# Performance work log

Measured on AMD Instinct MI355X. Metric: run time of the kernel, lower is better.

The kernel has to match this reference:

```python
import jax, jax.numpy as jnp
import numpy as np

# metaLinearLayer: per-sample weight W_b = left^T @ diag(meta_b) @ right.
# torch builds diag(meta)@eye@left then transposes and matmuls right, i.e.
# meta_weight[b] = (diag(meta_b) @ left).T @ right, shape (input_dim, out_dim).
# We apply it via associativity: (x @ left^T) * meta, then @ right -- same math,
# skipping the dense per-sample weight.

B, S, D_IN, D_OUT, P = 8, 4096, 2048, 2048, 256

def setup_inputs() -> dict:
    key = jax.random.key(0)
    ks = jax.random.split(key, 6)
    scale_l = (6.0 / D_IN) ** 0.5   # kaiming_uniform-ish magnitude
    scale_r = (6.0 / P) ** 0.5
    return {
        "input": jax.random.normal(ks[0], (B, S, D_IN), dtype=jnp.float32),
        "meta_input": jax.random.normal(ks[1], (B, P), dtype=jnp.float32),
        "left": jax.random.uniform(ks[2], (P, D_IN), dtype=jnp.float32, minval=-scale_l, maxval=scale_l),
        "right": jax.random.uniform(ks[3], (P, D_OUT), dtype=jnp.float32, minval=-scale_r, maxval=scale_r),
        "bias_w": jax.random.uniform(ks[4], (P, D_OUT), dtype=jnp.float32, minval=-scale_r, maxval=scale_r),
        "bias_b": jax.random.uniform(ks[5], (D_OUT,), dtype=jnp.float32, minval=-scale_r, maxval=scale_r),
    }

def reference(input, meta_input, left, right, bias_w, bias_b):
    # project input to rank-P space: [B,S,P]
    h = jnp.einsum('bsj,pj->bsp', input, left)
    # per-sample diagonal scaling by meta_input
    h = h * meta_input[:, None, :]
    # project to out_dim: [B,S,out_dim]
    out = jnp.einsum('bsp,pk->bsk', h, right)
    # meta bias = project2bias(meta_input), broadcast over seq
    meta_bias = meta_input @ bias_w + bias_b  # [B, out_dim]
    return out + meta_bias[:, None, :]
```

## Files before the change

### kernel.cpp

```cpp
#include <hip/hip_runtime.h>
#include <hip/hip_bf16.h>
#include <stdint.h>

#define B_    8
#define S_    4096
#define DIN   2048
#define DOUT  2048
#define P_    256
#define M_    (B_ * S_)

typedef __attribute__((ext_vector_type(4))) float f32x4;
typedef __attribute__((ext_vector_type(8))) short bf16x8;
typedef __attribute__((ext_vector_type(4))) short bf16x4;

static __device__ __forceinline__ short f2bs(float x) {
    __hip_bfloat16 h = __float2bfloat16(x);
    return *reinterpret_cast<short*>(&h);
}

static __device__ __forceinline__ void gld_lds16(const void* g, void* l) {
    __builtin_amdgcn_global_load_lds(
        (const __attribute__((address_space(1))) unsigned int*)(uintptr_t)g,
        (__attribute__((address_space(3))) unsigned int*)(uintptr_t)l,
        16, 0, 0);
}

#define SWZ(row, byteoff) ((byteoff) ^ (((row) & 7) << 4))

__global__ __launch_bounds__(256)
void cvt_left(const float* __restrict__ src, short* __restrict__ dst) {
    int i = blockIdx.x * 256 + threadIdx.x;
    const float4* s = reinterpret_cast<const float4*>(src) + (size_t)i * 2;
    float4 a = s[0], b = s[1];
    bf16x8 o;
    o[0]=f2bs(a.x); o[1]=f2bs(a.y); o[2]=f2bs(a.z); o[3]=f2bs(a.w);
    o[4]=f2bs(b.x); o[5]=f2bs(b.y); o[6]=f2bs(b.z); o[7]=f2bs(b.w);
    *(reinterpret_cast<bf16x8*>(dst) + i) = o;
}

__global__ __launch_bounds__(256)
void transposeR(const float* __restrict__ R, short* __restrict__ Rt) {
    __shared__ float T[64][65];
    const int n0 = blockIdx.x * 64;
    const int p0 = blockIdx.y * 64;
    const int tid = threadIdx.x;
    #pragma unroll
    for (int e = 0; e < 16; ++e) {
        int idx = tid + e * 256;
        int r = idx >> 6, c = idx & 63;
        T[r][c] = R[(size_t)(p0 + r) * DOUT + n0 + c];
    }
    __syncthreads();
    #pragma unroll
    for (int e = 0; e < 4; ++e) {
        int g = tid + e * 256;
        int n = g >> 4, p4 = (g & 15) << 2;
        bf16x4 v;
        v[0] = f2bs(T[p4 + 0][n]); v[1] = f2bs(T[p4 + 1][n]);
        v[2] = f2bs(T[p4 + 2][n]); v[3] = f2bs(T[p4 + 3][n]);
        *reinterpret_cast<bf16x4*>(&Rt[(size_t)(n0 + n) * P_ + p0 + p4]) = v;
    }
}

__global__ __launch_bounds__(256)
void meta_bias(const float* __restrict__ meta,
               const float* __restrict__ bias_w,
               const float* __restrict__ bias_b,
               float* __restrict__ mb) {
    int b = blockIdx.x >> 3;
    int k = (blockIdx.x & 7) * 256 + threadIdx.x;
    const float* mrow = meta + b * P_;
    float acc = bias_b[k];
    #pragma unroll 8
    for (int p = 0; p < P_; ++p)
        acc = fmaf(mrow[p], bias_w[(size_t)p * DOUT + k], acc);
    mb[(size_t)b * DOUT + k] = acc;
}

__global__ __launch_bounds__(256, 2)
void gemm1(const float* __restrict__ X, const short* __restrict__ Lb,
           const float* __restrict__ meta, char* __restrict__ Hsw) {
    __shared__ short As[2][64 * 64];

    const int tid  = threadIdx.x;
    const int lane = tid & 63;
    const int w    = tid >> 6;
    const int lm   = lane & 15;
    const int rg   = lane >> 4;
    const int mblk = blockIdx.x;
    const int r0   = mblk * 64;
    const int bidx = mblk >> 6;

    const int row_s = tid >> 2;
    const int kq    = (tid & 3) * 16;
    const float* xbase = X + (size_t)(r0 + row_s) * DIN + kq;
    const int wsw0 = SWZ(row_s, row_s * 128 + kq * 2);
    const int wsw1 = SWZ(row_s, row_s * 128 + kq * 2 + 16);

    f32x4 acc[4][4] = {};
    float4 xr0, xr1, xr2, xr3;
    {
        const float4* s = reinterpret_cast<const float4*>(xbase);
        xr0 = s[0]; xr1 = s[1]; xr2 = s[2]; xr3 = s[3];
    }

    for (int kt = 0; kt < 32; ++kt) {
        char* asb = (char*)As[kt & 1];
        bf16x8 o0, o1;
        o0[0]=f2bs(xr0.x); o0[1]=f2bs(xr0.y); o0[2]=f2bs(xr0.z); o0[3]=f2bs(xr0.w);
        o0[4]=f2bs(xr1.x); o0[5]=f2bs(xr1.y); o0[6]=f2bs(xr1.z); o0[7]=f2bs(xr1.w);
        o1[0]=f2bs(xr2.x); o1[1]=f2bs(xr2.y); o1[2]=f2bs(xr2.z); o1[3]=f2bs(xr2.w);
        o1[4]=f2bs(xr3.x); o1[5]=f2bs(xr3.y); o1[6]=f2bs(xr3.z); o1[7]=f2bs(xr3.w);
        *reinterpret_cast<bf16x8*>(asb + wsw0) = o0;
        *reinterpret_cast<bf16x8*>(asb + wsw1) = o1;
        __syncthreads();

        if (kt < 31) {
            const float4* s = reinterpret_cast<const float4*>(xbase + (kt + 1) * 64);
            xr0 = s[0]; xr1 = s[1]; xr2 = s[2]; xr3 = s[3];
        }

        bf16x8 bfr[4][2];
        #pragma unroll
        for (int j = 0; j < 4; ++j)
            #pragma unroll
            for (int kk = 0; kk < 2; ++kk)
                bfr[j][kk] = *reinterpret_cast<const bf16x8*>(
                    Lb + (size_t)(w * 64 + j * 16 + lm) * DIN + kt * 64 + kk * 32 + rg * 8);

        #pragma unroll
        for (int kk = 0; kk < 2; ++kk) {
            bf16x8 af[4];
            #pragma unroll
            for (int i = 0; i < 4; ++i) {
                int m = i * 16 + lm;
                af[i] = *reinterpret_cast<const bf16x8*>(
                    asb + SWZ(m, m * 128 + (kk * 32 + rg * 8) * 2));
            }
            #pragma unroll
            for (int i = 0; i < 4; ++i)
                #pragma unroll
                for (int j = 0; j < 4; ++j)
                    acc[i][j] = __builtin_amdgcn_mfma_f32_16x16x32_bf16(
                        af[i], bfr[j][kk], acc[i][j], 0, 0, 0);
        }
    }

    const float* mrow = meta + bidx * P_;
    char* hb = Hsw + (size_t)mblk * 32768 + w * 8192;
    float mv[4];
    #pragma unroll
    for (int j = 0; j < 4; ++j) mv[j] = mrow[w * 64 + j * 16 + lm];
    #pragma unroll
    for (int i = 0; i < 4; ++i) {
        #pragma unroll
        for (int j = 0; j < 4; ++j) {
            int kk2 = j * 16 + lm;
            #pragma unroll
            for (int q = 0; q < 4; ++q) {
                int r = i * 16 + rg * 4 + q;
                *reinterpret_cast<short*>(hb + SWZ(r, r * 128 + kk2 * 2)) =
                    f2bs(acc[i][j][q] * mv[j]);
            }
        }
    }
}

__global__ __launch_bounds__(256, 3)
void gemm2(const char* __restrict__ Hsw, const short* __restrict__ Rt,
           const float* __restrict__ mb, float* __restrict__ O) {
    __shared__ short As[64 * 64];

    const int tid  = threadIdx.x;
    const int lane = tid & 63;
    const int w    = tid >> 6;
    const int lm   = lane & 15;
    const int rg   = lane >> 4;
    const int mblk = blockIdx.x;
    const int r0   = mblk * 64;
    const int c0   = blockIdx.y * 256;
    const int bidx = mblk >> 6;
    char* asb = (char*)As;

    f32x4 acc[4][4] = {};

    for (int kt = 0; kt < 4; ++kt) {
        const char* aimg = Hsw + ((size_t)mblk * 4 + kt) * 8192;
        gld_lds16(aimg + (w * 2 + 0) * 1024 + lane * 16, asb + (w * 2 + 0) * 1024);
        gld_lds16(aimg + (w * 2 + 1) * 1024 + lane * 16, asb + (w * 2 + 1) * 1024);
        __syncthreads();

        bf16x8 bfr[4][2];
        #pragma unroll
        for (int j = 0; j < 4; ++j)
            #pragma unroll
            for (int kk = 0; kk < 2; ++kk)
                bfr[j][kk] = *reinterpret_cast<const bf16x8*>(
                    Rt + (size_t)(c0 + w * 64 + j * 16 + lm) * P_ + kt * 64 + kk * 32 + rg * 8);

        #pragma unroll
        for (int kk = 0; kk < 2; ++kk) {
            bf16x8 af[4];
            #pragma unroll
            for (int i = 0; i < 4; ++i) {
                int m = i * 16 + lm;
                af[i] = *reinterpret_cast<const bf16x8*>(
                    asb + SWZ(m, m * 128 + (kk * 32 + rg * 8) * 2));
            }
            #pragma unroll
            for (int i = 0; i < 4; ++i)
                #pragma unroll
                for (int j = 0; j < 4; ++j)
                    acc[i][j] = __builtin_amdgcn_mfma_f32_16x16x32_bf16(
                        af[i], bfr[j][kk], acc[i][j], 0, 0, 0);
        }
        __syncthreads();
    }

    const float* mbr = mb + (size_t)bidx * DOUT;
    float bv[4];
    #pragma unroll
    for (int j = 0; j < 4; ++j) bv[j] = mbr[c0 + w * 64 + j * 16 + lm];
    #pragma unroll
    for (int i = 0; i < 4; ++i) {
        #pragma unroll
        for (int j = 0; j < 4; ++j) {
            int col = c0 + w * 64 + j * 16 + lm;
            #pragma unroll
            for (int q = 0; q < 4; ++q) {
                int row = r0 + i * 16 + rg * 4 + q;
                O[(size_t)row * DOUT + col] = acc[i][j][q] + bv[j];
            }
        }
    }
}

extern "C" void kernel_launch(void* const* d_in, const int* in_sizes, int n_in,
                              void* d_out, int out_size, void* d_ws, size_t ws_size,
                              hipStream_t stream) {
    const float* input  = (const float*)d_in[0];
    const float* meta   = (const float*)d_in[1];
    const float* left   = (const float*)d_in[2];
    const float* right  = (const float*)d_in[3];
    const float* bias_w = (const float*)d_in[4];
    const float* bias_b = (const float*)d_in[5];
    float* out = (float*)d_out;

    char* ws  = (char*)d_ws;
    char* Hsw = ws;
    float* mb = (float*)(ws + 16777216);
    short* Lb = (short*)(ws + 16777216 + 65536);
    short* Rt = (short*)(ws + 16777216 + 65536 + 1048576);

    cvt_left  <<<256, 256, 0, stream>>>(left, Lb);
    transposeR<<<dim3(DOUT / 64, P_ / 64), 256, 0, stream>>>(right, Rt);
    meta_bias <<<64, 256, 0, stream>>>(meta, bias_w, bias_b, mb);

    gemm1<<<dim3(M_ / 64), 256, 0, stream>>>(input, Lb, meta, Hsw);
    gemm2<<<dim3(M_ / 64, DOUT / 256), 256, 0, stream>>>(Hsw, Rt, mb, out);
}
```

Baseline: 597.0 us.

## Fuse both GEMMs into one kernel keeping H in LDS, prepack weights as fragments

Merges gemm1 and gemm2 into a single kernel. Each 64-row block keeps its scaled rank-256 intermediate H in shared memory and then loops over all 2048 output columns, so H is no longer written to and read back from global memory. The left and right weights are pre-packed into MFMA fragment order so each lane's B-operand loads are contiguous. The trade-offs are fewer blocks (512 instead of 4096 for the second stage), 48KB of LDS per block, and a serial loop over the 8 output tiles.

```diff
diff --git a/kernel.cpp b/kernel.cpp
--- a/kernel.cpp
+++ b/kernel.cpp
@@ -11,35 +11,33 @@
 
 typedef __attribute__((ext_vector_type(4))) float f32x4;
 typedef __attribute__((ext_vector_type(8))) short bf16x8;
-typedef __attribute__((ext_vector_type(4))) short bf16x4;
 
 static __device__ __forceinline__ short f2bs(float x) {
     __hip_bfloat16 h = __float2bfloat16(x);
     return *reinterpret_cast<short*>(&h);
 }
 
-static __device__ __forceinline__ void gld_lds16(const void* g, void* l) {
-    __builtin_amdgcn_global_load_lds(
-        (const __attribute__((address_space(1))) unsigned int*)(uintptr_t)g,
-        (__attribute__((address_space(3))) unsigned int*)(uintptr_t)l,
-        16, 0, 0);
-}
-
 #define SWZ(row, byteoff) ((byteoff) ^ (((row) & 7) << 4))
 
 __global__ __launch_bounds__(256)
-void cvt_left(const float* __restrict__ src, short* __restrict__ dst) {
-    int i = blockIdx.x * 256 + threadIdx.x;
-    const float4* s = reinterpret_cast<const float4*>(src) + (size_t)i * 2;
-    float4 a = s[0], b = s[1];
+void prep_Lfrag(const float* __restrict__ L, short* __restrict__ Lf) {
+    int g = blockIdx.x * 256 + threadIdx.x;
+    int p  = g >> 8;
+    int c8 = g & 255;
+    int k  = c8 * 8;
+    int kt = k >> 6, kk = (k >> 5) & 1, rg = (k >> 3) & 3;
+    const float* src = L + (size_t)p * DIN + k;
+    float4 v0 = *reinterpret_cast<const float4*>(src);
+    float4 v1 = *reinterpret_cast<const float4*>(src + 4);
     bf16x8 o;
-    o[0]=f2bs(a.x); o[1]=f2bs(a.y); o[2]=f2bs(a.z); o[3]=f2bs(a.w);
-    o[4]=f2bs(b.x); o[5]=f2bs(b.y); o[6]=f2bs(b.z); o[7]=f2bs(b.w);
-    *(reinterpret_cast<bf16x8*>(dst) + i) = o;
+    o[0]=f2bs(v0.x); o[1]=f2bs(v0.y); o[2]=f2bs(v0.z); o[3]=f2bs(v0.w);
+    o[4]=f2bs(v1.x); o[5]=f2bs(v1.y); o[6]=f2bs(v1.z); o[7]=f2bs(v1.w);
+    size_t idx16 = ((((size_t)(p >> 4) * 32 + kt) * 2 + kk) * 4 + rg) * 16 + (p & 15);
+    reinterpret_cast<bf16x8*>(Lf)[idx16] = o;
 }
 
 __global__ __launch_bounds__(256)
-void transposeR(const float* __restrict__ R, short* __restrict__ Rt) {
+void prep_Rfrag(const float* __restrict__ R, short* __restrict__ Rf) {
     __shared__ float T[64][65];
     const int n0 = blockIdx.x * 64;
     const int p0 = blockIdx.y * 64;
@@ -52,13 +50,18 @@
     }
     __syncthreads();
     #pragma unroll
-    for (int e = 0; e < 4; ++e) {
-        int g = tid + e * 256;
-        int n = g >> 4, p4 = (g & 15) << 2;
-        bf16x4 v;
-        v[0] = f2bs(T[p4 + 0][n]); v[1] = f2bs(T[p4 + 1][n]);
-        v[2] = f2bs(T[p4 + 2][n]); v[3] = f2bs(T[p4 + 3][n]);
-        *reinterpret_cast<bf16x4*>(&Rt[(size_t)(n0 + n) * P_ + p0 + p4]) = v;
+    for (int e = 0; e < 2; ++e) {
+        int q  = tid + e * 256;
+        int nl = q >> 3;
+        int pg = q & 7;
+        bf16x8 o;
+        #pragma unroll
+        for (int u = 0; u < 8; ++u) o[u] = f2bs(T[pg * 8 + u][nl]);
+        int n = n0 + nl;
+        int pglob = p0 + pg * 8;
+        int kt = pglob >> 6, kk = (pglob >> 5) & 1, rg = (pglob >> 3) & 3;
+        size_t idx16 = ((((size_t)(n >> 4) * 4 + kt) * 2 + kk) * 4 + rg) * 16 + (n & 15);
+        reinterpret_cast<bf16x8*>(Rf)[idx16] = o;
     }
 }
 
@@ -78,9 +81,11 @@
 }
 
 __global__ __launch_bounds__(256, 2)
-void gemm1(const float* __restrict__ X, const short* __restrict__ Lb,
-           const float* __restrict__ meta, char* __restrict__ Hsw) {
+void fused(const float* __restrict__ X, const short* __restrict__ Lf,
+           const short* __restrict__ Rf, const float* __restrict__ meta,
+           const float* __restrict__ mb, float* __restrict__ O) {
     __shared__ short As[2][64 * 64];
+    __shared__ short Ht[4][64 * 64];
 
     const int tid  = threadIdx.x;
     const int lane = tid & 63;
@@ -90,6 +95,9 @@
     const int mblk = blockIdx.x;
     const int r0   = mblk * 64;
     const int bidx = mblk >> 6;
+
+    const bf16x8* Lf8 = reinterpret_cast<const bf16x8*>(Lf);
+    const bf16x8* Rf8 = reinterpret_cast<const bf16x8*>(Rf);
 
     const int row_s = tid >> 2;
     const int kq    = (tid & 3) * 16;
@@ -125,8 +133,8 @@
         for (int j = 0; j < 4; ++j)
             #pragma unroll
             for (int kk = 0; kk < 2; ++kk)
-                bfr[j][kk] = *reinterpret_cast<const bf16x8*>(
-                    Lb + (size_t)(w * 64 + j * 16 + lm) * DIN + kt * 64 + kk * 32 + rg * 8);
+                bfr[j][kk] = Lf8[((((size_t)(w * 4 + j) * 32 + kt) * 2 + kk) * 4) * 16
+                                 + rg * 16 + lm];
 
         #pragma unroll
         for (int kk = 0; kk < 2; ++kk) {
@@ -146,90 +154,69 @@
         }
     }
 
-    const float* mrow = meta + bidx * P_;
-    char* hb = Hsw + (size_t)mblk * 32768 + w * 8192;
-    float mv[4];
-    #pragma unroll
-    for (int j = 0; j < 4; ++j) mv[j] = mrow[w * 64 + j * 16 + lm];
-    #pragma unroll
-    for (int i = 0; i < 4; ++i) {
+    {
+        const float* mrow = meta + bidx * P_;
+        char* hb = (char*)Ht[w];
+        float mv[4];
+        #pragma unroll
+        for (int j = 0; j < 4; ++j) mv[j] = mrow[w * 64 + j * 16 + lm];
+        #pragma unroll
+        for (int i = 0; i < 4; ++i) {
+            #pragma unroll
+            for (int j = 0; j < 4; ++j) {
+                int kk2 = j * 16 + lm;
+                #pragma unroll
+                for (int q = 0; q < 4; ++q) {
+                    int r = i * 16 + rg * 4 + q;
+                    *reinterpret_cast<short*>(hb + SWZ(r, r * 128 + kk2 * 2)) =
+                        f2bs(acc[i][j][q] * mv[j]);
+                }
+            }
+        }
+    }
+    __syncthreads();
+
+    const float* mbr = mb + (size_t)bidx * DOUT;
+    for (int nb = 0; nb < 8; ++nb) {
+        f32x4 acc2[4][4] = {};
+        #pragma unroll
+        for (int kt2 = 0; kt2 < 4; ++kt2) {
+            bf16x8 bfr2[4][2];
+            #pragma unroll
+            for (int j = 0; j < 4; ++j)
+                #pragma unroll
+                for (int kk = 0; kk < 2; ++kk)
+                    bfr2[j][kk] = Rf8[((((size_t)(nb * 16 + w * 4 + j) * 4 + kt2) * 2 + kk) * 4) * 16
+                                      + rg * 16 + lm];
+            const char* hsb = (const char*)Ht[kt2];
+            #pragma unroll
+            for (int kk = 0; kk < 2; ++kk) {
+                bf16x8 af[4];
+                #pragma unroll
+                for (int i = 0; i < 4; ++i) {
+                    int m = i * 16 + lm;
+                    af[i] = *reinterpret_cast<const bf16x8*>(
+                        hsb + SWZ(m, m * 128 + (kk * 32 + rg * 8) * 2));
+                }
+                #pragma unroll
+                for (int i = 0; i < 4; ++i)
+                    #pragma unroll
+                    for (int j = 0; j < 4; ++j)
+                        acc2[i][j] = __builtin_amdgcn_mfma_f32_16x16x32_bf16(
+                            af[i], bfr2[j][kk], acc2[i][j], 0, 0, 0);
+            }
+        }
         #pragma unroll
         for (int j = 0; j < 4; ++j) {
-            int kk2 = j * 16 + lm;
-            #pragma unroll
-            for (int q = 0; q < 4; ++q) {
-                int r = i * 16 + rg * 4 + q;
-                *reinterpret_cast<short*>(hb + SWZ(r, r * 128 + kk2 * 2)) =
-                    f2bs(acc[i][j][q] * mv[j]);
-            }
-        }
-    }
-}
-
-__global__ __launch_bounds__(256, 3)
-void gemm2(const char* __restrict__ Hsw, const short* __restrict__ Rt,
-           const float* __restrict__ mb, float* __restrict__ O) {
-    __shared__ short As[64 * 64];
-
-    const int tid  = threadIdx.x;
-    const int lane = tid & 63;
-    const int w    = tid >> 6;
-    const int lm   = lane & 15;
-    const int rg   = lane >> 4;
-    const int mblk = blockIdx.x;
-    const int r0   = mblk * 64;
-    const int c0   = blockIdx.y * 256;
-    const int bidx = mblk >> 6;
-    char* asb = (char*)As;
-
-    f32x4 acc[4][4] = {};
-
-    for (int kt = 0; kt < 4; ++kt) {
-        const char* aimg = Hsw + ((size_t)mblk * 4 + kt) * 8192;
-        gld_lds16(aimg + (w * 2 + 0) * 1024 + lane * 16, asb + (w * 2 + 0) * 1024);
-        gld_lds16(aimg + (w * 2 + 1) * 1024 + lane * 16, asb + (w * 2 + 1) * 1024);
-        __syncthreads();
-
-        bf16x8 bfr[4][2];
-        #pragma unroll
-        for (int j = 0; j < 4; ++j)
-            #pragma unroll
-            for (int kk = 0; kk < 2; ++kk)
-                bfr[j][kk] = *reinterpret_cast<const bf16x8*>(
-                    Rt + (size_t)(c0 + w * 64 + j * 16 + lm) * P_ + kt * 64 + kk * 32 + rg * 8);
-
-        #pragma unroll
-        for (int kk = 0; kk < 2; ++kk) {
-            bf16x8 af[4];
+            int col = nb * 256 + w * 64 + j * 16 + lm;
+            float bv = mbr[col];
             #pragma unroll
             for (int i = 0; i < 4; ++i) {
-                int m = i * 16 + lm;
-                af[i] = *reinterpret_cast<const bf16x8*>(
-                    asb + SWZ(m, m * 128 + (kk * 32 + rg * 8) * 2));
-            }
-            #pragma unroll
-            for (int i = 0; i < 4; ++i)
-                #pragma unroll
-                for (int j = 0; j < 4; ++j)
-                    acc[i][j] = __builtin_amdgcn_mfma_f32_16x16x32_bf16(
-                        af[i], bfr[j][kk], acc[i][j], 0, 0, 0);
-        }
-        __syncthreads();
-    }
-
-    const float* mbr = mb + (size_t)bidx * DOUT;
-    float bv[4];
-    #pragma unroll
-    for (int j = 0; j < 4; ++j) bv[j] = mbr[c0 + w * 64 + j * 16 + lm];
-    #pragma unroll
-    for (int i = 0; i < 4; ++i) {
-        #pragma unroll
-        for (int j = 0; j < 4; ++j) {
-            int col = c0 + w * 64 + j * 16 + lm;
-            #pragma unroll
-            for (int q = 0; q < 4; ++q) {
-                int row = r0 + i * 16 + rg * 4 + q;
-                O[(size_t)row * DOUT + col] = acc[i][j][q] + bv[j];
+                #pragma unroll
+                for (int q = 0; q < 4; ++q) {
+                    int row = r0 + i * 16 + rg * 4 + q;
+                    O[(size_t)row * DOUT + col] = acc2[i][j][q] + bv;
+                }
             }
         }
     }
@@ -247,15 +234,13 @@
     float* out = (float*)d_out;
 
     char* ws  = (char*)d_ws;
-    char* Hsw = ws;
-    float* mb = (float*)(ws + 16777216);
-    short* Lb = (short*)(ws + 16777216 + 65536);
-    short* Rt = (short*)(ws + 16777216 + 65536 + 1048576);
-
-    cvt_left  <<<256, 256, 0, stream>>>(left, Lb);
-    transposeR<<<dim3(DOUT / 64, P_ / 64), 256, 0, stream>>>(right, Rt);
+    float* mb = (float*)ws;
+    short* Lf = (short*)(ws + 65536);
+    short* Rf = (short*)(ws + 65536 + 1048576);
+
+    prep_Lfrag<<<256, 256, 0, stream>>>(left, Lf);
+    prep_Rfrag<<<dim3(DOUT / 64, P_ / 64), 256, 0, stream>>>(right, Rf);
     meta_bias <<<64, 256, 0, stream>>>(meta, bias_w, bias_b, mb);
 
-    gemm1<<<dim3(M_ / 64), 256, 0, stream>>>(input, Lb, meta, Hsw);
-    gemm2<<<dim3(M_ / 64, DOUT / 256), 256, 0, stream>>>(Hsw, Rt, mb, out);
-}
+    fused<<<dim3(M_ / 64), 256, 0, stream>>>(input, Lf, Rf, meta, mb, out);
+}
```

After: 572.8 us. 4.0% less time.
